# Optimization experiments

Hardware: AMD Instinct MI355X
Metric: run time of the kernel (lower is better)

The kernel has to match this reference:

```python
import jax, jax.numpy as jnp
import numpy as np

B_SZ, SEQ, D_MODEL, D_STATE, DT_RANK = 2, 2048, 1024, 16, 64


def setup_inputs() -> dict:
    key = jax.random.key(0)
    ks = jax.random.split(key, 7)
    x = jax.random.normal(ks[0], (B_SZ, SEQ, D_MODEL), dtype=jnp.float32)
    dt_proj_input = jax.random.normal(ks[1], (B_SZ, SEQ, DT_RANK), dtype=jnp.float32)
    # A_log initialized as -log(arange(1, d_state+1)) per _initialize_parameters
    A_log = -jnp.log(jnp.arange(1, D_STATE + 1, dtype=jnp.float32))
    # dt_proj: weight ~ N(0, 0.1), bias = log(expm1(dt)) - 2 with dt ~ logU(dt_min, dt_max)
    dt_W = 0.1 * jax.random.normal(ks[2], (D_MODEL, DT_RANK), dtype=jnp.float32)
    u = jax.random.uniform(ks[3], (D_MODEL,), dtype=jnp.float32)
    dt = jnp.exp(u * (np.log(0.1) - np.log(0.001)) + np.log(0.001))
    dt = jnp.clip(dt, 0.0001, None)
    dt_b = jnp.log(jnp.expm1(dt)) - 2.0
    # B_proj / C_proj: xavier-uniform (d_state, d_model), no bias
    lim = np.sqrt(6.0 / (D_STATE + D_MODEL)).astype(np.float32)
    B_W = jax.random.uniform(ks[4], (D_STATE, D_MODEL), dtype=jnp.float32, minval=-lim, maxval=lim)
    C_W = jax.random.uniform(ks[5], (D_STATE, D_MODEL), dtype=jnp.float32, minval=-lim, maxval=lim)
    D_vec = jnp.ones((D_MODEL,), dtype=jnp.float32)
    return {"x": x, "dt_proj_input": dt_proj_input, "A_log": A_log,
            "dt_W": dt_W, "dt_b": dt_b, "B_W": B_W, "C_W": C_W, "D_vec": D_vec}


def reference(x, dt_proj_input, A_log, dt_W, dt_b, B_W, C_W, D_vec):
    # dt = softplus(Linear(dt_proj_input) + bias)  -- note bias is added twice, faithful to source
    dt = jax.nn.softplus(jnp.einsum('blr,dr->bld', dt_proj_input, dt_W) + 2.0 * dt_b)  # (b,l,d)
    Bm = jnp.einsum('bld,nd->bln', x, B_W)  # (b,l,n)
    Cm = jnp.einsum('bld,nd->bln', x, C_W)  # (b,l,n)
    A = -jnp.exp(A_log)                      # (n,)
    dA = jnp.exp(dt[..., None] * A)                                   # (b,l,d,n)
    dB = dt[..., None] * Bm[:, :, None, :] * x[..., None]             # (b,l,d,n)
    # linear recurrence h[t] = dA[t] * h[t-1] + dB[t]
    def step(h, ab):
        a, b = ab
        h = a * h + b
        return h, h
    h0 = jnp.zeros((x.shape[0], x.shape[2], A_log.shape[0]), dtype=x.dtype)
    _, states = jax.lax.scan(step, h0, (jnp.swapaxes(dA, 0, 1), jnp.swapaxes(dB, 0, 1)))
    states = jnp.swapaxes(states, 0, 1)      # (b,l,d,n)
    y = jnp.einsum('bldn,bln->bld', states, Cm)
    return y + x * D_vec
```

## Files before the change

kernel.cpp:

```cpp
#include <hip/hip_runtime.h>

#define LOG2E 1.44269504088896340736f
#define LN2   0.69314718055994530942f

constexpr int BSZ = 2, SEQ = 2048, DM = 1024, DS = 16, DR = 64;
constexpr int NC = 64, CL = SEQ / NC;

constexpr size_t OFF_DT   = 0;
constexpr size_t OFF_BM   = OFF_DT + (size_t)BSZ*SEQ*DM;
constexpr size_t OFF_CM   = OFF_BM + (size_t)BSZ*SEQ*DS;
constexpr size_t OFF_S    = OFF_CM + (size_t)BSZ*SEQ*DS;
constexpr size_t OFF_HEND = OFF_S  + (size_t)BSZ*NC*DM;
constexpr size_t OFF_HIN  = OFF_HEND + (size_t)BSZ*NC*DS*DM;
constexpr size_t OFF_PART = OFF_HEND;

__device__ inline float softplusf(float z) {
  float e = __builtin_amdgcn_exp2f(z * LOG2E);
  if (z > 15.f) return z;
  if (z < -8.f) return e;
  return __builtin_amdgcn_logf(1.f + e) * LN2;
}

__device__ inline void fma4(float& acc, float4 a, float4 b) {
  acc = fmaf(a.x, b.x, fmaf(a.y, b.y, fmaf(a.z, b.z, fmaf(a.w, b.w, acc))));
}

__global__ __launch_bounds__(256, 3) void k_dtproj(const float* __restrict__ inp,
                                                   const float* __restrict__ W,
                                                   const float* __restrict__ bias,
                                                   float* __restrict__ dt) {
  __shared__ __align__(16) float At[64][66];
  __shared__ __align__(16) float Wt[64][130];
  int mt = blockIdx.x >> 3, nt = blockIdx.x & 7;
  int m0 = mt * 64, n0 = nt * 128;
  int t = threadIdx.x;
#pragma unroll
  for (int i = 0; i < 4; ++i) {
    int idx4 = t + 256 * i;
    int m = idx4 >> 4, k4 = (idx4 & 15) * 4;
    float4 v = *(const float4*)&inp[(size_t)(m0 + m) * DR + k4];
    At[k4 + 0][m] = v.x; At[k4 + 1][m] = v.y; At[k4 + 2][m] = v.z; At[k4 + 3][m] = v.w;
  }
#pragma unroll
  for (int i = 0; i < 8; ++i) {
    int idx4 = t + 256 * i;
    int n = idx4 >> 4, k4 = (idx4 & 15) * 4;
    float4 v = *(const float4*)&W[(size_t)(n0 + n) * DR + k4];
    Wt[k4 + 0][n] = v.x; Wt[k4 + 1][n] = v.y; Wt[k4 + 2][n] = v.z; Wt[k4 + 3][n] = v.w;
  }
  __syncthreads();
  int mg = t >> 4, ng = t & 15;
  float acc[4][8] = {};
#pragma unroll 4
  for (int k = 0; k < 64; ++k) {
    float2 a01 = *(const float2*)&At[k][mg * 4];
    float2 a23 = *(const float2*)&At[k][mg * 4 + 2];
    float a[4] = {a01.x, a01.y, a23.x, a23.y};
    float w[8];
#pragma unroll
    for (int u = 0; u < 4; ++u) {
      float2 wv = *(const float2*)&Wt[k][ng * 8 + 2 * u];
      w[2 * u] = wv.x; w[2 * u + 1] = wv.y;
    }
#pragma unroll
    for (int i = 0; i < 4; ++i)
#pragma unroll
      for (int j = 0; j < 8; ++j)
        acc[i][j] = fmaf(a[i], w[j], acc[i][j]);
  }
  float bb[8];
  *(float4*)&bb[0] = *(const float4*)&bias[n0 + ng * 8];
  *(float4*)&bb[4] = *(const float4*)&bias[n0 + ng * 8 + 4];
#pragma unroll
  for (int i = 0; i < 4; ++i) {
    int m = m0 + mg * 4 + i;
    float o[8];
#pragma unroll
    for (int j = 0; j < 8; ++j) o[j] = softplusf(acc[i][j] + 2.f * bb[j]);
    *(float4*)&dt[(size_t)m * DM + n0 + ng * 8]     = make_float4(o[0], o[1], o[2], o[3]);
    *(float4*)&dt[(size_t)m * DM + n0 + ng * 8 + 4] = make_float4(o[4], o[5], o[6], o[7]);
  }
}

__global__ __launch_bounds__(256) void k_bcm_part(const float* __restrict__ x,
                                                  const float* __restrict__ BW,
                                                  const float* __restrict__ CW,
                                                  float* __restrict__ part) {
  __shared__ __align__(16) float xt[64][132];
  __shared__ __align__(16) float wt[32][132];
  int mt = blockIdx.x >> 3, ks = blockIdx.x & 7;
  int m0 = mt * 64, k0 = ks * 128;
  int t = threadIdx.x;
#pragma unroll
  for (int i = 0; i < 8; ++i) {
    int idx4 = t + 256 * i;
    int r = idx4 >> 5, c4 = idx4 & 31;
    float4 v = *(const float4*)&x[(size_t)(m0 + r) * DM + k0 + c4 * 4];
    *(float4*)&xt[r][c4 * 4] = v;
  }
#pragma unroll
  for (int i = 0; i < 4; ++i) {
    int idx4 = t + 256 * i;
    int n = idx4 >> 5, c4 = idx4 & 31;
    const float* src = (n < 16) ? &BW[(size_t)n * DM + k0 + c4 * 4]
                                : &CW[(size_t)(n - 16) * DM + k0 + c4 * 4];
    *(float4*)&wt[n][c4 * 4] = *(const float4*)src;
  }
  __syncthreads();
  int lg = t >> 3, ng = t & 7;
  float acc[2][4] = {};
#pragma unroll 4
  for (int k4 = 0; k4 < 32; ++k4) {
    float4 xa0 = *(const float4*)&xt[lg * 2 + 0][k4 * 4];
    float4 xa1 = *(const float4*)&xt[lg * 2 + 1][k4 * 4];
#pragma unroll
    for (int j = 0; j < 4; ++j) {
      float4 w = *(const float4*)&wt[ng * 4 + j][k4 * 4];
      fma4(acc[0][j], xa0, w);
      fma4(acc[1][j], xa1, w);
    }
  }
#pragma unroll
  for (int i = 0; i < 2; ++i) {
    float4 o = make_float4(acc[i][0], acc[i][1], acc[i][2], acc[i][3]);
    *(float4*)&part[(size_t)ks * (4096 * 32) + (size_t)(m0 + lg * 2 + i) * 32 + ng * 4] = o;
  }
}

__global__ __launch_bounds__(256) void k_bcm_reduce(const float* __restrict__ part,
                                                    float* __restrict__ Bm,
                                                    float* __restrict__ Cm) {
#pragma unroll
  for (int i = 0; i < 4; ++i) {
    int id = blockIdx.x * 1024 + threadIdx.x + 256 * i;
    float s = 0.f;
#pragma unroll
    for (int ks = 0; ks < 8; ++ks) s += part[(size_t)ks * (4096 * 32) + id];
    int bl = id >> 5, n = id & 31;
    if (n < 16) Bm[(size_t)bl * DS + n] = s;
    else        Cm[(size_t)bl * DS + (n - 16)] = s;
  }
}

__global__ __launch_bounds__(256) void k_phase1(const float* __restrict__ x,
                                                const float* __restrict__ dt,
                                                const float* __restrict__ Bm,
                                                const float* __restrict__ A_log,
                                                float* __restrict__ Ssum,
                                                float* __restrict__ hend) {
  __shared__ float bml[CL * DS];
  int bid = blockIdx.x;
  int b = bid >> 8, rem = bid & 255;
  int c = rem >> 2, dg = rem & 3;
  int t = threadIdx.x;
  int d = dg * 256 + t;
  const float* bsrc = Bm + ((size_t)b * SEQ + c * CL) * DS;
  *(float2*)&bml[t * 2] = *(const float2*)&bsrc[t * 2];
  __syncthreads();
  float a2[16];
#pragma unroll
  for (int n = 0; n < 16; ++n)
    a2[n] = -__builtin_amdgcn_exp2f(A_log[n] * LOG2E) * LOG2E;
  float h[16] = {};
  float S = 0.f;
  size_t base = ((size_t)b * SEQ + c * CL) * DM + d;
#pragma unroll 2
  for (int l = 0; l < CL; ++l) {
    float dtv = dt[base + (size_t)l * DM];
    float xv  = x[base + (size_t)l * DM];
    S += dtv;
    float dtx = dtv * xv;
#pragma unroll
    for (int n = 0; n < 16; ++n) {
      float a = __builtin_amdgcn_exp2f(dtv * a2[n]);
      h[n] = fmaf(a, h[n], dtx * bml[l * DS + n]);
    }
  }
  size_t cc = (size_t)b * NC + c;
  Ssum[cc * DM + d] = S;
#pragma unroll
  for (int n = 0; n < 16; ++n) hend[(cc * DS + n) * DM + d] = h[n];
}

__global__ __launch_bounds__(256) void k_phase2(const float* __restrict__ A_log,
                                                const float* __restrict__ Ssum,
                                                const float* __restrict__ hend,
                                                float* __restrict__ hin) {
  int bid = blockIdx.x;
  int b = bid >> 6, rem = bid & 63;
  int n = rem >> 2, dg = rem & 3;
  int d = dg * 256 + threadIdx.x;
  float a2 = -__builtin_amdgcn_exp2f(A_log[n] * LOG2E) * LOG2E;
  float h = 0.f;
  for (int c = 0; c < NC; ++c) {
    size_t cc = (size_t)b * NC + c;
    hin[(cc * DS + n) * DM + d] = h;
    float aa = __builtin_amdgcn_exp2f(a2 * Ssum[cc * DM + d]);
    h = fmaf(aa, h, hend[(cc * DS + n) * DM + d]);
  }
}

__global__ __launch_bounds__(256) void k_phase3(const float* __restrict__ x,
                                                const float* __restrict__ dt,
                                                const float* __restrict__ Bm,
                                                const float* __restrict__ Cm,
                                                const float* __restrict__ A_log,
                                                const float* __restrict__ Dvec,
                                                const float* __restrict__ hin,
                                                float* __restrict__ out) {
  __shared__ float bml[CL * DS], cml[CL * DS];
  int bid = blockIdx.x;
  int b = bid >> 8, rem = bid & 255;
  int c = rem >> 2, dg = rem & 3;
  int t = threadIdx.x;
  int d = dg * 256 + t;
  const float* bsrc = Bm + ((size_t)b * SEQ + c * CL) * DS;
  const float* csrc = Cm + ((size_t)b * SEQ + c * CL) * DS;
  *(float2*)&bml[t * 2] = *(const float2*)&bsrc[t * 2];
  *(float2*)&cml[t * 2] = *(const float2*)&csrc[t * 2];
  __syncthreads();
  float a2[16];
#pragma unroll
  for (int n = 0; n < 16; ++n)
    a2[n] = -__builtin_amdgcn_exp2f(A_log[n] * LOG2E) * LOG2E;
  size_t cc = (size_t)b * NC + c;
  float h[16];
#pragma unroll
  for (int n = 0; n < 16; ++n) h[n] = hin[(cc * DS + n) * DM + d];
  float dv = Dvec[d];
  size_t base = ((size_t)b * SEQ + c * CL) * DM + d;
#pragma unroll 2
  for (int l = 0; l < CL; ++l) {
    float dtv = dt[base + (size_t)l * DM];
    float xv  = x[base + (size_t)l * DM];
    float dtx = dtv * xv;
    float y = 0.f;
#pragma unroll
    for (int n = 0; n < 16; ++n) {
      float a = __builtin_amdgcn_exp2f(dtv * a2[n]);
      h[n] = fmaf(a, h[n], dtx * bml[l * DS + n]);
      y = fmaf(h[n], cml[l * DS + n], y);
    }
    out[base + (size_t)l * DM] = fmaf(xv, dv, y);
  }
}

extern "C" void kernel_launch(void* const* d_in, const int* in_sizes, int n_in,
                              void* d_out, int out_size, void* d_ws, size_t ws_size,
                              hipStream_t stream) {
  (void)in_sizes; (void)n_in; (void)out_size; (void)ws_size;
  const float* x     = (const float*)d_in[0];
  const float* dtp   = (const float*)d_in[1];
  const float* A_log = (const float*)d_in[2];
  const float* dtW   = (const float*)d_in[3];
  const float* dtb   = (const float*)d_in[4];
  const float* BW    = (const float*)d_in[5];
  const float* CW    = (const float*)d_in[6];
  const float* Dv    = (const float*)d_in[7];
  float* out = (float*)d_out;
  float* ws  = (float*)d_ws;

  float* dt   = ws + OFF_DT;
  float* Bm   = ws + OFF_BM;
  float* Cm   = ws + OFF_CM;
  float* S    = ws + OFF_S;
  float* hend = ws + OFF_HEND;
  float* hin  = ws + OFF_HIN;
  float* part = ws + OFF_PART;

  k_dtproj    <<<512,  256, 0, stream>>>(dtp, dtW, dtb, dt);
  k_bcm_part  <<<512,  256, 0, stream>>>(x, BW, CW, part);
  k_bcm_reduce<<<128,  256, 0, stream>>>(part, Bm, Cm);
  k_phase1    <<<512,  256, 0, stream>>>(x, dt, Bm, A_log, S, hend);
  k_phase2    <<<128,  256, 0, stream>>>(A_log, S, hend, hin);
  k_phase3    <<<512,  256, 0, stream>>>(x, dt, Bm, Cm, A_log, Dv, hin, out);
}
```

Baseline: 77.61 us.

## Fuse dt and B/C projections into one launch, fold reduce into phase1

Merges the dt projection GEMM and the B/C partial GEMM into a single heterogeneous kernel, with the dt GEMM retiled to 128x128 tiles and 8x8 register blocking. The B/C split-K reduction now happens inside phase1, which writes Bm/Cm for phase3, so the separate reduce launch goes away. The partial buffer gets its own workspace region so it no longer aliases hend. Scan loop unroll factors are also raised. The aim is fewer launches and less launch/tail overhead, at the cost of larger register tiles and the partial buffer being read redundantly by four d-group blocks.

```diff
diff --git a/kernel.cpp b/kernel.cpp
--- a/kernel.cpp
+++ b/kernel.cpp
@@ -12,7 +12,7 @@
 constexpr size_t OFF_S    = OFF_CM + (size_t)BSZ*SEQ*DS;
 constexpr size_t OFF_HEND = OFF_S  + (size_t)BSZ*NC*DM;
 constexpr size_t OFF_HIN  = OFF_HEND + (size_t)BSZ*NC*DS*DM;
-constexpr size_t OFF_PART = OFF_HEND;
+constexpr size_t OFF_PART = OFF_HIN  + (size_t)BSZ*NC*DS*DM;
 
 __device__ inline float softplusf(float z) {
   float e = __builtin_amdgcn_exp2f(z * LOG2E);
@@ -25,127 +25,124 @@
   acc = fmaf(a.x, b.x, fmaf(a.y, b.y, fmaf(a.z, b.z, fmaf(a.w, b.w, acc))));
 }
 
-__global__ __launch_bounds__(256, 3) void k_dtproj(const float* __restrict__ inp,
-                                                   const float* __restrict__ W,
-                                                   const float* __restrict__ bias,
-                                                   float* __restrict__ dt) {
-  __shared__ __align__(16) float At[64][66];
-  __shared__ __align__(16) float Wt[64][130];
-  int mt = blockIdx.x >> 3, nt = blockIdx.x & 7;
-  int m0 = mt * 64, n0 = nt * 128;
-  int t = threadIdx.x;
-#pragma unroll
-  for (int i = 0; i < 4; ++i) {
-    int idx4 = t + 256 * i;
-    int m = idx4 >> 4, k4 = (idx4 & 15) * 4;
-    float4 v = *(const float4*)&inp[(size_t)(m0 + m) * DR + k4];
-    At[k4 + 0][m] = v.x; At[k4 + 1][m] = v.y; At[k4 + 2][m] = v.z; At[k4 + 3][m] = v.w;
-  }
-#pragma unroll
-  for (int i = 0; i < 8; ++i) {
-    int idx4 = t + 256 * i;
-    int n = idx4 >> 4, k4 = (idx4 & 15) * 4;
-    float4 v = *(const float4*)&W[(size_t)(n0 + n) * DR + k4];
-    Wt[k4 + 0][n] = v.x; Wt[k4 + 1][n] = v.y; Wt[k4 + 2][n] = v.z; Wt[k4 + 3][n] = v.w;
-  }
-  __syncthreads();
-  int mg = t >> 4, ng = t & 15;
-  float acc[4][8] = {};
-#pragma unroll 4
-  for (int k = 0; k < 64; ++k) {
-    float2 a01 = *(const float2*)&At[k][mg * 4];
-    float2 a23 = *(const float2*)&At[k][mg * 4 + 2];
-    float a[4] = {a01.x, a01.y, a23.x, a23.y};
-    float w[8];
-#pragma unroll
-    for (int u = 0; u < 4; ++u) {
-      float2 wv = *(const float2*)&Wt[k][ng * 8 + 2 * u];
-      w[2 * u] = wv.x; w[2 * u + 1] = wv.y;
-    }
-#pragma unroll
-    for (int i = 0; i < 4; ++i)
-#pragma unroll
-      for (int j = 0; j < 8; ++j)
-        acc[i][j] = fmaf(a[i], w[j], acc[i][j]);
-  }
-  float bb[8];
-  *(float4*)&bb[0] = *(const float4*)&bias[n0 + ng * 8];
-  *(float4*)&bb[4] = *(const float4*)&bias[n0 + ng * 8 + 4];
-#pragma unroll
-  for (int i = 0; i < 4; ++i) {
-    int m = m0 + mg * 4 + i;
-    float o[8];
-#pragma unroll
-    for (int j = 0; j < 8; ++j) o[j] = softplusf(acc[i][j] + 2.f * bb[j]);
-    *(float4*)&dt[(size_t)m * DM + n0 + ng * 8]     = make_float4(o[0], o[1], o[2], o[3]);
-    *(float4*)&dt[(size_t)m * DM + n0 + ng * 8 + 4] = make_float4(o[4], o[5], o[6], o[7]);
-  }
-}
-
-__global__ __launch_bounds__(256) void k_bcm_part(const float* __restrict__ x,
+__global__ __launch_bounds__(256, 2) void k_front(const float* __restrict__ inp,
+                                                  const float* __restrict__ W,
+                                                  const float* __restrict__ bias,
+                                                  float* __restrict__ dt,
+                                                  const float* __restrict__ x,
                                                   const float* __restrict__ BW,
                                                   const float* __restrict__ CW,
                                                   float* __restrict__ part) {
-  __shared__ __align__(16) float xt[64][132];
-  __shared__ __align__(16) float wt[32][132];
-  int mt = blockIdx.x >> 3, ks = blockIdx.x & 7;
-  int m0 = mt * 64, k0 = ks * 128;
+  __shared__ __align__(16) float smem[16896];
+  int bid = blockIdx.x;
   int t = threadIdx.x;
-#pragma unroll
-  for (int i = 0; i < 8; ++i) {
-    int idx4 = t + 256 * i;
-    int r = idx4 >> 5, c4 = idx4 & 31;
-    float4 v = *(const float4*)&x[(size_t)(m0 + r) * DM + k0 + c4 * 4];
-    *(float4*)&xt[r][c4 * 4] = v;
-  }
-#pragma unroll
-  for (int i = 0; i < 4; ++i) {
-    int idx4 = t + 256 * i;
-    int n = idx4 >> 5, c4 = idx4 & 31;
-    const float* src = (n < 16) ? &BW[(size_t)n * DM + k0 + c4 * 4]
-                                : &CW[(size_t)(n - 16) * DM + k0 + c4 * 4];
-    *(float4*)&wt[n][c4 * 4] = *(const float4*)src;
-  }
-  __syncthreads();
-  int lg = t >> 3, ng = t & 7;
-  float acc[2][4] = {};
-#pragma unroll 4
-  for (int k4 = 0; k4 < 32; ++k4) {
-    float4 xa0 = *(const float4*)&xt[lg * 2 + 0][k4 * 4];
-    float4 xa1 = *(const float4*)&xt[lg * 2 + 1][k4 * 4];
-#pragma unroll
-    for (int j = 0; j < 4; ++j) {
-      float4 w = *(const float4*)&wt[ng * 4 + j][k4 * 4];
-      fma4(acc[0][j], xa0, w);
-      fma4(acc[1][j], xa1, w);
-    }
-  }
-#pragma unroll
-  for (int i = 0; i < 2; ++i) {
-    float4 o = make_float4(acc[i][0], acc[i][1], acc[i][2], acc[i][3]);
-    *(float4*)&part[(size_t)ks * (4096 * 32) + (size_t)(m0 + lg * 2 + i) * 32 + ng * 4] = o;
-  }
-}
-
-__global__ __launch_bounds__(256) void k_bcm_reduce(const float* __restrict__ part,
-                                                    float* __restrict__ Bm,
-                                                    float* __restrict__ Cm) {
-#pragma unroll
-  for (int i = 0; i < 4; ++i) {
-    int id = blockIdx.x * 1024 + threadIdx.x + 256 * i;
-    float s = 0.f;
-#pragma unroll
-    for (int ks = 0; ks < 8; ++ks) s += part[(size_t)ks * (4096 * 32) + id];
-    int bl = id >> 5, n = id & 31;
-    if (n < 16) Bm[(size_t)bl * DS + n] = s;
-    else        Cm[(size_t)bl * DS + (n - 16)] = s;
+  if (bid < 256) {
+    float* At = smem;
+    float* Wt = smem + 64 * 132;
+    int mt = bid >> 3, nt = bid & 7;
+    int m0 = mt * 128, n0 = nt * 128;
+#pragma unroll
+    for (int i = 0; i < 8; ++i) {
+      int idx4 = t + 256 * i;
+      int m = idx4 >> 4, k4 = (idx4 & 15) * 4;
+      float4 v = *(const float4*)&inp[(size_t)(m0 + m) * DR + k4];
+      At[(k4 + 0) * 132 + m] = v.x; At[(k4 + 1) * 132 + m] = v.y;
+      At[(k4 + 2) * 132 + m] = v.z; At[(k4 + 3) * 132 + m] = v.w;
+    }
+#pragma unroll
+    for (int i = 0; i < 8; ++i) {
+      int idx4 = t + 256 * i;
+      int n = idx4 >> 4, k4 = (idx4 & 15) * 4;
+      float4 v = *(const float4*)&W[(size_t)(n0 + n) * DR + k4];
+      Wt[(k4 + 0) * 132 + n] = v.x; Wt[(k4 + 1) * 132 + n] = v.y;
+      Wt[(k4 + 2) * 132 + n] = v.z; Wt[(k4 + 3) * 132 + n] = v.w;
+    }
+    __syncthreads();
+    int mg = t >> 4, ng = t & 15;
+    float acc[8][8] = {};
+#pragma unroll 4
+    for (int k = 0; k < 64; ++k) {
+      const float* rowA = At + k * 132;
+      const float* rowW = Wt + k * 132;
+      float4 a0 = *(const float4*)&rowA[mg * 8];
+      float4 a1 = *(const float4*)&rowA[mg * 8 + 4];
+      float4 w0 = *(const float4*)&rowW[ng * 4];
+      float4 w1 = *(const float4*)&rowW[ng * 4 + 64];
+      float a[8] = {a0.x, a0.y, a0.z, a0.w, a1.x, a1.y, a1.z, a1.w};
+      float w[8] = {w0.x, w0.y, w0.z, w0.w, w1.x, w1.y, w1.z, w1.w};
+#pragma unroll
+      for (int i = 0; i < 8; ++i)
+#pragma unroll
+        for (int j = 0; j < 8; ++j)
+          acc[i][j] = fmaf(a[i], w[j], acc[i][j]);
+    }
+    float4 b0 = *(const float4*)&bias[n0 + ng * 4];
+    float4 b1 = *(const float4*)&bias[n0 + ng * 4 + 64];
+    float bb[8] = {b0.x, b0.y, b0.z, b0.w, b1.x, b1.y, b1.z, b1.w};
+#pragma unroll
+    for (int i = 0; i < 8; ++i) {
+      int m = m0 + mg * 8 + i;
+      float4 lo, hi;
+      lo.x = softplusf(acc[i][0] + 2.f * bb[0]);
+      lo.y = softplusf(acc[i][1] + 2.f * bb[1]);
+      lo.z = softplusf(acc[i][2] + 2.f * bb[2]);
+      lo.w = softplusf(acc[i][3] + 2.f * bb[3]);
+      hi.x = softplusf(acc[i][4] + 2.f * bb[4]);
+      hi.y = softplusf(acc[i][5] + 2.f * bb[5]);
+      hi.z = softplusf(acc[i][6] + 2.f * bb[6]);
+      hi.w = softplusf(acc[i][7] + 2.f * bb[7]);
+      *(float4*)&dt[(size_t)m * DM + n0 + ng * 4]      = lo;
+      *(float4*)&dt[(size_t)m * DM + n0 + ng * 4 + 64] = hi;
+    }
+  } else {
+    float* xt = smem;
+    float* wt = smem + 64 * 132;
+    int bid2 = bid - 256;
+    int mt = bid2 >> 3, ks = bid2 & 7;
+    int m0 = mt * 64, k0 = ks * 128;
+#pragma unroll
+    for (int i = 0; i < 8; ++i) {
+      int idx4 = t + 256 * i;
+      int r = idx4 >> 5, c4 = (idx4 & 31) * 4;
+      float4 v = *(const float4*)&x[(size_t)(m0 + r) * DM + k0 + c4];
+      *(float4*)&xt[r * 132 + c4] = v;
+    }
+#pragma unroll
+    for (int i = 0; i < 4; ++i) {
+      int idx4 = t + 256 * i;
+      int n = idx4 >> 5, c4 = (idx4 & 31) * 4;
+      const float* src = (n < 16) ? &BW[(size_t)n * DM + k0 + c4]
+                                  : &CW[(size_t)(n - 16) * DM + k0 + c4];
+      *(float4*)&wt[n * 132 + c4] = *(const float4*)src;
+    }
+    __syncthreads();
+    int lg = t >> 3, ng = t & 7;
+    float acc[2][4] = {};
+#pragma unroll 4
+    for (int k4 = 0; k4 < 32; ++k4) {
+      float4 xa0 = *(const float4*)&xt[(lg * 2 + 0) * 132 + k4 * 4];
+      float4 xa1 = *(const float4*)&xt[(lg * 2 + 1) * 132 + k4 * 4];
+#pragma unroll
+      for (int j = 0; j < 4; ++j) {
+        float4 w = *(const float4*)&wt[(ng + 8 * j) * 132 + k4 * 4];
+        fma4(acc[0][j], xa0, w);
+        fma4(acc[1][j], xa1, w);
+      }
+    }
+#pragma unroll
+    for (int i = 0; i < 2; ++i)
+#pragma unroll
+      for (int j = 0; j < 4; ++j)
+        part[(size_t)ks * (4096 * 32) + (size_t)(m0 + lg * 2 + i) * 32 + ng + 8 * j] = acc[i][j];
   }
 }
 
 __global__ __launch_bounds__(256) void k_phase1(const float* __restrict__ x,
                                                 const float* __restrict__ dt,
-                                                const float* __restrict__ Bm,
+                                                const float* __restrict__ part,
                                                 const float* __restrict__ A_log,
+                                                float* __restrict__ Bm,
+                                                float* __restrict__ Cm,
                                                 float* __restrict__ Ssum,
                                                 float* __restrict__ hend) {
   __shared__ float bml[CL * DS];
@@ -154,8 +151,27 @@
   int c = rem >> 2, dg = rem & 3;
   int t = threadIdx.x;
   int d = dg * 256 + t;
-  const float* bsrc = Bm + ((size_t)b * SEQ + c * CL) * DS;
-  *(float2*)&bml[t * 2] = *(const float2*)&bsrc[t * 2];
+  size_t blbase = (size_t)b * SEQ + c * CL;
+  {
+    size_t e = (blbase + (t >> 3)) * 32 + 2 * (t & 7);
+    float2 s = make_float2(0.f, 0.f);
+#pragma unroll
+    for (int ks = 0; ks < 8; ++ks) {
+      float2 v = *(const float2*)&part[(size_t)ks * (4096 * 32) + e];
+      s.x += v.x; s.y += v.y;
+    }
+    *(float2*)&bml[t * 2] = s;
+    if (dg == 0) {
+      *(float2*)&Bm[(blbase + (t >> 3)) * DS + 2 * (t & 7)] = s;
+      float2 sc = make_float2(0.f, 0.f);
+#pragma unroll
+      for (int ks = 0; ks < 8; ++ks) {
+        float2 v = *(const float2*)&part[(size_t)ks * (4096 * 32) + e + 16];
+        sc.x += v.x; sc.y += v.y;
+      }
+      *(float2*)&Cm[(blbase + (t >> 3)) * DS + 2 * (t & 7)] = sc;
+    }
+  }
   __syncthreads();
   float a2[16];
 #pragma unroll
@@ -163,8 +179,8 @@
     a2[n] = -__builtin_amdgcn_exp2f(A_log[n] * LOG2E) * LOG2E;
   float h[16] = {};
   float S = 0.f;
-  size_t base = ((size_t)b * SEQ + c * CL) * DM + d;
-#pragma unroll 2
+  size_t base = blbase * DM + d;
+#pragma unroll 4
   for (int l = 0; l < CL; ++l) {
     float dtv = dt[base + (size_t)l * DM];
     float xv  = x[base + (size_t)l * DM];
@@ -192,6 +208,7 @@
   int d = dg * 256 + threadIdx.x;
   float a2 = -__builtin_amdgcn_exp2f(A_log[n] * LOG2E) * LOG2E;
   float h = 0.f;
+#pragma unroll 8
   for (int c = 0; c < NC; ++c) {
     size_t cc = (size_t)b * NC + c;
     hin[(cc * DS + n) * DM + d] = h;
@@ -229,7 +246,7 @@
   for (int n = 0; n < 16; ++n) h[n] = hin[(cc * DS + n) * DM + d];
   float dv = Dvec[d];
   size_t base = ((size_t)b * SEQ + c * CL) * DM + d;
-#pragma unroll 2
+#pragma unroll 4
   for (int l = 0; l < CL; ++l) {
     float dtv = dt[base + (size_t)l * DM];
     float xv  = x[base + (size_t)l * DM];
@@ -268,10 +285,8 @@
   float* hin  = ws + OFF_HIN;
   float* part = ws + OFF_PART;
 
-  k_dtproj    <<<512,  256, 0, stream>>>(dtp, dtW, dtb, dt);
-  k_bcm_part  <<<512,  256, 0, stream>>>(x, BW, CW, part);
-  k_bcm_reduce<<<128,  256, 0, stream>>>(part, Bm, Cm);
-  k_phase1    <<<512,  256, 0, stream>>>(x, dt, Bm, A_log, S, hend);
-  k_phase2    <<<128,  256, 0, stream>>>(A_log, S, hend, hin);
-  k_phase3    <<<512,  256, 0, stream>>>(x, dt, Bm, Cm, A_log, Dv, hin, out);
-}
+  k_front <<<768, 256, 0, stream>>>(dtp, dtW, dtb, dt, x, BW, CW, part);
+  k_phase1<<<512, 256, 0, stream>>>(x, dt, part, A_log, Bm, Cm, S, hend);
+  k_phase2<<<128, 256, 0, stream>>>(A_log, S, hend, hin);
+  k_phase3<<<512, 256, 0, stream>>>(x, dt, Bm, Cm, A_log, Dv, hin, out);
+}
```

Result: faster. 64.40 us (-17.0%).
